# Optimization experiments

Hardware: AMD Instinct MI355X
Metric: run time of the kernel (lower is better)

Reference implementation:

```python
import jax, jax.numpy as jnp
import numpy as np
from jax import lax

B, N, D, H = 8, 2048, 512, 1024


def setup_inputs() -> dict:
    key = jax.random.key(0)
    k0, k1, k2 = jax.random.split(key, 3)
    x = jax.random.normal(k0, (B, N, D), jnp.float32)
    conv_w = jax.random.normal(k1, (H, D, 3), jnp.float32) * (1.0 / np.sqrt(3 * D))
    conv_b = jnp.zeros((H,), jnp.float32)
    ln_g = jnp.ones((H,), jnp.float32)
    ln_b = jnp.zeros((H,), jnp.float32)
    proj_w = jax.random.normal(k2, (H, 2), jnp.float32) * (1.0 / np.sqrt(H))
    proj_b = jnp.zeros((2,), jnp.float32)
    return dict(x=x, conv_w=conv_w, conv_b=conv_b, ln_g=ln_g, ln_b=ln_b,
                proj_w=proj_w, proj_b=proj_b)


def reference(x, conv_w, conv_b, ln_g, ln_b, proj_w, proj_b):
    b, n, _ = x.shape
    # Conv1d(input_dim->hidden, k=3, pad=1) on [B, C, N]
    h = lax.conv_general_dilated(x.transpose(0, 2, 1), conv_w, (1,), [(1, 1)],
                                 dimension_numbers=('NCH', 'OIH', 'NCH'))
    h = h.transpose(0, 2, 1) + conv_b          # [B, N, H]
    h = jax.nn.relu(h)
    # LayerNorm over hidden dim (dropout is identity at inference)
    mu = jnp.mean(h, axis=-1, keepdims=True)
    var = jnp.mean((h - mu) ** 2, axis=-1, keepdims=True)
    h = (h - mu) * lax.rsqrt(var + 1e-5) * ln_g + ln_b
    groups_probs = h @ proj_w + proj_b          # [B, N, 2]

    g = jnp.argmax(groups_probs, axis=-1)       # [B, N] in {0,1}
    pos = jnp.arange(n)
    base = (pos + 1).astype(jnp.float32)        # 1..N
    # col 0 forced 0; start positions (g==1, pos>0) forced 0
    zero_mask = (pos[None, :] == 0) | ((g == 1) & (pos[None, :] > 0))
    vals = jnp.where(zero_mask, 0.0, jnp.broadcast_to(base[None, :], (b, n)))
    vals = vals.at[:, -1].set(float(n))         # last col = N (overrides zeroing)
    # stable descending sort by nonzero-ness == stable ascending sort by (val==0)
    order = jnp.argsort((vals == 0.0).astype(jnp.int32), axis=1)
    groups = jnp.take_along_axis(vals, order, axis=1)[:, :, None]  # [B, N, 1]

    t = base[None, None, :]                     # [1, 1, N], values 1..N
    # row 0: 1[t <= groups[:,0]]
    row0 = jnp.clip(groups[:, 0, :][:, None, :] - t + 1.0, 0.0, 1.0)      # [B, 1, N]
    # rows 1..: 1[groups[:,i-1] < t <= groups[:,i]]
    rest = (jnp.clip(groups[:, 1:, :] - t + 1.0, 0.0, 1.0)
            * jnp.clip(t - groups[:, :-1, :], 0.0, 1.0))                   # [B, N-1, N]
    grouping_matrix = jnp.concatenate([row0, rest], axis=1)                # [B, N, N]
    return (groups_probs, grouping_matrix)
```

## Files before the change

kernel.cpp:

```cpp
#include <hip/hip_runtime.h>

#define Bsz 8
#define Nsz 2048
#define Dsz 512
#define Hsz 1024
#define K3D 1536

typedef __attribute__((ext_vector_type(8))) short short8;
typedef __attribute__((ext_vector_type(4))) float f32x4;

static __device__ __forceinline__ unsigned short f2bf(float f) {
    unsigned u = __builtin_bit_cast(unsigned, f);
    unsigned r = (u + 0x7FFFu + ((u >> 16) & 1u)) >> 16;
    return (unsigned short)r;
}
static __device__ __forceinline__ float bf2f(unsigned short u) {
    return __builtin_bit_cast(float, (unsigned)u << 16);
}
static __device__ __forceinline__ void gld16(const void* g, void* l) {
    __builtin_amdgcn_global_load_lds(
        (const __attribute__((address_space(1))) void*)g,
        (__attribute__((address_space(3))) void*)l, 16, 0, 0);
}


__global__ __launch_bounds__(256) void prep_kernel(
    const float* __restrict__ cw, unsigned short* __restrict__ wsh,
    unsigned short* __restrict__ wsl,
    const float* __restrict__ lng, const float* __restrict__ lnb,
    const float* __restrict__ pw, float* __restrict__ CD,
    float* __restrict__ gq0, float* __restrict__ gq1)
{
    __shared__ float red[4][4];
    int blk = blockIdx.x, tid = threadIdx.x;
    if (blk < 192) {
        int gid = blk * 256 + tid;
        int s = gid >> 10, h = gid & 1023;
        int t = s >> 4, c = s & 15;
        const float* src = cw + (size_t)h * K3D + (size_t)c * 96 + t;
        short hv[32], lv[32];
        #pragma unroll
        for (int j = 0; j < 32; ++j) {
            float v = src[3 * j];
            unsigned short hi = f2bf(v);
            hv[j] = (short)hi;
            lv[j] = (short)f2bf(v - bf2f(hi));
        }
        #pragma unroll
        for (int m = 0; m < 4; ++m) {
            size_t dst = (((size_t)s * 4 + m) * 1024 + h) * 16;
            *(short8*)((char*)wsh + dst) = *(short8*)&hv[m * 8];
            *(short8*)((char*)wsl + dst) = *(short8*)&lv[m * 8];
        }
    } else if (blk == 192) {
        float c0 = 0.f, c1 = 0.f, d0 = 0.f, d1 = 0.f;
        for (int h = tid; h < Hsz; h += 256) {
            float g = lng[h], b = lnb[h];
            float w0 = pw[2 * h], w1 = pw[2 * h + 1];
            c0 = fmaf(g, w0, c0); c1 = fmaf(g, w1, c1);
            d0 = fmaf(b, w0, d0); d1 = fmaf(b, w1, d1);
        }
        #pragma unroll
        for (int m = 32; m >= 1; m >>= 1) {
            c0 += __shfl_xor(c0, m, 64); c1 += __shfl_xor(c1, m, 64);
            d0 += __shfl_xor(d0, m, 64); d1 += __shfl_xor(d1, m, 64);
        }
        int w = tid >> 6;
        if ((tid & 63) == 0) { red[w][0] = c0; red[w][1] = c1; red[w][2] = d0; red[w][3] = d1; }
        __syncthreads();
        if (tid == 0) {
            CD[0] = red[0][0] + red[1][0] + red[2][0] + red[3][0];
            CD[1] = red[0][1] + red[1][1] + red[2][1] + red[3][1];
            CD[2] = red[0][2] + red[1][2] + red[2][2] + red[3][2];
            CD[3] = red[0][3] + red[1][3] + red[2][3] + red[3][3];
        }
    } else {
        int h = (blk - 193) * 256 + tid;
        float g = lng[h];
        gq0[h] = g * pw[2 * h];
        gq1[h] = g * pw[2 * h + 1];
    }
}

__global__ __launch_bounds__(256) void convert_x_kernel(
    const float* __restrict__ x, unsigned short* __restrict__ xsh,
    unsigned short* __restrict__ xsl)
{
    int tid = threadIdx.x;
    int r = blockIdx.x * 4 + (tid >> 6);
    int e = tid & 63;
    int b  = r / 2050;
    int rp = r - b * 2050;
    int c  = e >> 2;
    int qq = e & 3;
    size_t dst = ((((size_t)b * 16 + c) * 4 + qq) * 2050 + rp) * 16;
    short8 hv, lv;
    if (rp == 0 || rp == 2049) {
        #pragma unroll
        for (int u = 0; u < 8; ++u) { hv[u] = 0; lv[u] = 0; }
    } else {
        const float* p = x + ((size_t)b * Nsz + (rp - 1)) * Dsz + e * 8;
        float4 v0 = *(const float4*)p;
        float4 v1 = *(const float4*)(p + 4);
        float vv[8] = { v0.x, v0.y, v0.z, v0.w, v1.x, v1.y, v1.z, v1.w };
        #pragma unroll
        for (int u = 0; u < 8; ++u) {
            unsigned short h = f2bf(vv[u]);
            hv[u] = (short)h;
            lv[u] = (short)f2bf(vv[u] - bf2f(h));
        }
    }
    *(short8*)((char*)xsh + dst) = hv;
    *(short8*)((char*)xsl + dst) = lv;
}

__global__ __launch_bounds__(256, 2) void gemm10_kernel(
    const unsigned short* __restrict__ xsh, const unsigned short* __restrict__ xsl,
    const unsigned short* __restrict__ wsh, const unsigned short* __restrict__ wsl,
    const float* __restrict__ cb, const float* __restrict__ gq0,
    const float* __restrict__ gq1, float* __restrict__ part)
{
    __shared__ __align__(16) char lds[32768];

    int tid = threadIdx.x;
    int swz = (blockIdx.x & 7) * 128 + (blockIdx.x >> 3);
    int mt  = swz >> 3;
    int ntb = swz & 7;
    int bb  = mt >> 4;
    int n0  = (mt & 15) * 128;
    int n0c = ntb * 128;
    int n0g = bb * Nsz + n0;

    int l = tid & 63, w = tid >> 6;
    int wr = w >> 1, wc = w & 1;
    int r = l & 15, qq = l >> 4;

    int boff_r = qq * 2048 + (wc * 64 + r) * 16;
    int ldsBw  = w * 2048;

    const char* pBh = (const char*)wsh + w * 16384 + (size_t)(n0c + l) * 16;
    const char* pBl = (const char*)wsl + w * 16384 + (size_t)(n0c + l) * 16;

    const char* pAh = (const char*)xsh + (size_t)bb * 2099200 + qq * 32800
                    + (size_t)(n0 + wr * 64 + r) * 16;
    const char* pAl = (const char*)xsl + (size_t)bb * 2099200 + qq * 32800
                    + (size_t)(n0 + wr * 64 + r) * 16;

    f32x4 acc[4][4];
    #pragma unroll
    for (int i = 0; i < 4; ++i)
        #pragma unroll
        for (int j = 0; j < 4; ++j) acc[i][j] = (f32x4){0.f, 0.f, 0.f, 0.f};

    short8 a0h[4], a0l[4], a1h[4], a1l[4];

#define AOFF(sn) ((size_t)(((sn) & 15) * 131200 + ((sn) >> 4) * 16))
#define LOADA(AH, AL, sn) do { size_t ao = AOFF(sn);                           \
    _Pragma("unroll") for (int f = 0; f < 4; ++f) {                            \
        AH[f] = *(const short8*)(pAh + ao + f * 256);                          \
        AL[f] = *(const short8*)(pAl + ao + f * 256); } } while (0)

#define STAGEB(lb, sn) do { size_t bo = (size_t)(sn) * 65536;                  \
    gld16(pBh + bo,        (lb) + ldsBw);                                      \
    gld16(pBh + bo + 1024, (lb) + ldsBw + 1024);                               \
    gld16(pBl + bo,        (lb) + 8192 + ldsBw);                               \
    gld16(pBl + bo + 1024, (lb) + 8192 + ldsBw + 1024); } while (0)

#define COMPUTE(buf, AH, AL) do {                                              \
    short8 bh[4], bl[4];                                                       \
    _Pragma("unroll") for (int j = 0; j < 4; ++j) {                            \
        bh[j] = *(const short8*)((buf) + boff_r + j * 256);                    \
        bl[j] = *(const short8*)((buf) + 8192 + boff_r + j * 256); }           \
    __builtin_amdgcn_s_setprio(1);                                             \
    _Pragma("unroll") for (int i = 0; i < 4; ++i)                              \
        _Pragma("unroll") for (int j = 0; j < 4; ++j) {                        \
            acc[i][j] = __builtin_amdgcn_mfma_f32_16x16x32_bf16(AH[i], bh[j], acc[i][j], 0, 0, 0); \
            acc[i][j] = __builtin_amdgcn_mfma_f32_16x16x32_bf16(AH[i], bl[j], acc[i][j], 0, 0, 0); \
            acc[i][j] = __builtin_amdgcn_mfma_f32_16x16x32_bf16(AL[i], bh[j], acc[i][j], 0, 0, 0); } \
    __builtin_amdgcn_s_setprio(0);                                             \
} while (0)

    LOADA(a0h, a0l, 0);
    STAGEB(lds, 0);

    for (int sp = 0; sp < 24; ++sp) {
        int s1 = sp * 2 + 1;
        LOADA(a1h, a1l, s1);
        STAGEB(lds + 16384, s1);
        asm volatile("s_waitcnt vmcnt(12)" ::: "memory");
        __builtin_amdgcn_s_barrier();
        asm volatile("" ::: "memory");
        COMPUTE(lds, a0h, a0l);
        __builtin_amdgcn_s_barrier();
        if (s1 < 47) {
            LOADA(a0h, a0l, s1 + 1);
            STAGEB(lds, s1 + 1);
            asm volatile("s_waitcnt vmcnt(12)" ::: "memory");
        } else {
            asm volatile("s_waitcnt vmcnt(0)" ::: "memory");
        }
        __builtin_amdgcn_s_barrier();
        asm volatile("" ::: "memory");
        COMPUTE(lds + 16384, a1h, a1l);
        __builtin_amdgcn_s_barrier();
    }
#undef AOFF
#undef LOADA
#undef STAGEB
#undef COMPUTE

    float cbv[4], g0v[4], g1v[4];
    #pragma unroll
    for (int j = 0; j < 4; ++j) {
        int col = n0c + wc * 64 + j * 16 + r;
        cbv[j] = cb[col]; g0v[j] = gq0[col]; g1v[j] = gq1[col];
    }
    int slot = ntb * 8 + wc * 4;
    #pragma unroll
    for (int i = 0; i < 4; ++i) {
        #pragma unroll
        for (int reg = 0; reg < 4; ++reg) {
            float v0 = 0.f, v2 = 0.f, va = 0.f, vb = 0.f;
            #pragma unroll
            for (int j = 0; j < 4; ++j) {
                float v = acc[i][j][reg] + cbv[j];
                v = fmaxf(v, 0.f);
                v0 += v;
                v2 = fmaf(v, v, v2);
                va = fmaf(v, g0v[j], va);
                vb = fmaf(v, g1v[j], vb);
            }
            #pragma unroll
            for (int msk = 1; msk < 16; msk <<= 1) {
                v0 += __shfl_xor(v0, msk, 64); v2 += __shfl_xor(v2, msk, 64);
                va += __shfl_xor(va, msk, 64); vb += __shfl_xor(vb, msk, 64);
            }
            if (r == 0) {
                int rowg = n0g + wr * 64 + i * 16 + qq * 4 + reg;
                *(f32x4*)(part + (size_t)rowg * 64 + slot) = (f32x4){v0, v2, va, vb};
            }
        }
    }
}

__global__ __launch_bounds__(256) void probs_kernel(
    const float* __restrict__ part, const float* __restrict__ CD,
    const float* __restrict__ pb, float* __restrict__ probs,
    int* __restrict__ gout)
{
    int row = blockIdx.x * 256 + threadIdx.x;
    float S0 = 0.f, S2 = 0.f, Sa = 0.f, Sb = 0.f;
    const float4* p = (const float4*)(part + (size_t)row * 64);
    #pragma unroll
    for (int c = 0; c < 16; ++c) {
        float4 v = p[c];
        S0 += v.x; S2 += v.y; Sa += v.z; Sb += v.w;
    }
    float mu  = S0 * (1.0f / Hsz);
    float var = S2 * (1.0f / Hsz) - mu * mu;
    float rsq = 1.0f / sqrtf(var + 1e-5f);
    float p0 = fmaf(rsq, Sa - mu * CD[0], CD[2] + pb[0]);
    float p1 = fmaf(rsq, Sb - mu * CD[1], CD[3] + pb[1]);
    probs[(size_t)row * 2]     = p0;
    probs[(size_t)row * 2 + 1] = p1;
    gout[row] = (p1 > p0) ? 1 : 0;
}

#define ROWS 64
#define CCH 128
#define NCC (Hsz / CCH)
#define DSTEP 32

__global__ __launch_bounds__(256) void consts_kernel(
    const float* __restrict__ lng, const float* __restrict__ lnb,
    const float* __restrict__ pw, float* __restrict__ CD)
{
    int tid = threadIdx.x;
    float c0 = 0.f, c1 = 0.f, d0 = 0.f, d1 = 0.f;
    for (int h = tid; h < Hsz; h += 256) {
        float g = lng[h], b = lnb[h];
        float w0 = pw[2 * h], w1 = pw[2 * h + 1];
        c0 = fmaf(g, w0, c0); c1 = fmaf(g, w1, c1);
        d0 = fmaf(b, w0, d0); d1 = fmaf(b, w1, d1);
    }
    #pragma unroll
    for (int m = 32; m >= 1; m >>= 1) {
        c0 += __shfl_xor(c0, m, 64); c1 += __shfl_xor(c1, m, 64);
        d0 += __shfl_xor(d0, m, 64); d1 += __shfl_xor(d1, m, 64);
    }
    __shared__ float red[4][4];
    int w = tid >> 6;
    if ((tid & 63) == 0) { red[w][0] = c0; red[w][1] = c1; red[w][2] = d0; red[w][3] = d1; }
    __syncthreads();
    if (tid == 0) {
        CD[0] = red[0][0] + red[1][0] + red[2][0] + red[3][0];
        CD[1] = red[0][1] + red[1][1] + red[2][1] + red[3][1];
        CD[2] = red[0][2] + red[1][2] + red[2][2] + red[3][2];
        CD[3] = red[0][3] + red[1][3] + red[2][3] + red[3][3];
    }
}

__global__ __launch_bounds__(256) void conv_ln_proj_kernel(
    const float* __restrict__ x, const float* __restrict__ cw,
    const float* __restrict__ cb, const float* __restrict__ lng,
    const float* __restrict__ pw, const float* __restrict__ pb,
    const float* __restrict__ CD, float* __restrict__ probs,
    int* __restrict__ gout)
{
    __shared__ float Xl[DSTEP][66];
    __shared__ float Bl[3][DSTEP][CCH];
    __shared__ float Sl[ROWS][4];

    int tid = threadIdx.x;
    int blk = blockIdx.x;
    int b  = blk >> 5;
    int n0 = (blk & 31) * ROWS;
    int rg = tid >> 5;
    int cg = tid & 31;
    int sr = tid >> 2;
    int sq = tid & 3;
    const float* xb = x + (size_t)b * Nsz * Dsz;

    float s0[8], s2[8], sa[8], sb[8];
    #pragma unroll
    for (int i = 0; i < 8; ++i) { s0[i] = 0.f; s2[i] = 0.f; sa[i] = 0.f; sb[i] = 0.f; }

    for (int cc = 0; cc < NCC; ++cc) {
        float cbv[4], gq0[4], gq1[4];
        {
            int hb = cc * CCH + cg * 4;
            #pragma unroll
            for (int j = 0; j < 4; ++j) {
                int h = hb + j;
                cbv[j] = cb[h];
                float gg = lng[h];
                gq0[j] = gg * pw[2 * h];
                gq1[j] = gg * pw[2 * h + 1];
            }
        }
        float acc[8][4];
        #pragma unroll
        for (int i = 0; i < 8; ++i)
            #pragma unroll
            for (int j = 0; j < 4; ++j) acc[i][j] = 0.f;

        for (int ds = 0; ds < Dsz / DSTEP; ++ds) {
            int d0 = ds * DSTEP;
            __syncthreads();
            {
                int n = n0 - 1 + sr;
                float4 v0 = make_float4(0.f, 0.f, 0.f, 0.f), v1 = v0;
                if ((unsigned)n < (unsigned)Nsz) {
                    const float* p = xb + (size_t)n * Dsz + d0 + sq * 8;
                    v0 = *(const float4*)p;
                    v1 = *(const float4*)(p + 4);
                }
                int dd = sq * 8;
                Xl[dd + 0][sr] = v0.x; Xl[dd + 1][sr] = v0.y;
                Xl[dd + 2][sr] = v0.z; Xl[dd + 3][sr] = v0.w;
                Xl[dd + 4][sr] = v1.x; Xl[dd + 5][sr] = v1.y;
                Xl[dd + 6][sr] = v1.z; Xl[dd + 7][sr] = v1.w;
                if (tid < 8) {
                    int r2 = 64 + (tid >> 2);
                    int q2 = tid & 3;
                    int n2 = n0 - 1 + r2;
                    float4 u0 = make_float4(0.f, 0.f, 0.f, 0.f), u1 = u0;
                    if ((unsigned)n2 < (unsigned)Nsz) {
                        const float* p2 = xb + (size_t)n2 * Dsz + d0 + q2 * 8;
                        u0 = *(const float4*)p2;
                        u1 = *(const float4*)(p2 + 4);
                    }
                    int dd2 = q2 * 8;
                    Xl[dd2 + 0][r2] = u0.x; Xl[dd2 + 1][r2] = u0.y;
                    Xl[dd2 + 2][r2] = u0.z; Xl[dd2 + 3][r2] = u0.w;
                    Xl[dd2 + 4][r2] = u1.x; Xl[dd2 + 5][r2] = u1.y;
                    Xl[dd2 + 6][r2] = u1.z; Xl[dd2 + 7][r2] = u1.w;
                }
            }
            {
                int hl = tid >> 1;
                int half = tid & 1;
                const float* p = cw + (size_t)(cc * CCH + hl) * K3D + (size_t)d0 * 3 + half * 48;
                #pragma unroll
                for (int mq = 0; mq < 12; ++mq) {
                    float4 v = *(const float4*)(p + mq * 4);
                    float vv[4] = { v.x, v.y, v.z, v.w };
                    #pragma unroll
                    for (int e = 0; e < 4; ++e) {
                        int c  = mq * 4 + e;
                        int dl = half * 16 + c / 3;
                        int kk = c % 3;
                        Bl[kk][dl][hl] = vv[e];
                    }
                }
            }
            __syncthreads();
            #pragma unroll 4
            for (int dd = 0; dd < DSTEP; ++dd) {
                float a[10];
                #pragma unroll
                for (int j = 0; j < 10; ++j) a[j] = Xl[dd][rg * 8 + j];
                #pragma unroll
                for (int kk = 0; kk < 3; ++kk) {
                    float4 bv = *(const float4*)&Bl[kk][dd][cg * 4];
                    #pragma unroll
                    for (int i = 0; i < 8; ++i) {
                        float av = a[i + kk];
                        acc[i][0] = fmaf(av, bv.x, acc[i][0]);
                        acc[i][1] = fmaf(av, bv.y, acc[i][1]);
                        acc[i][2] = fmaf(av, bv.z, acc[i][2]);
                        acc[i][3] = fmaf(av, bv.w, acc[i][3]);
                    }
                }
            }
        }
        #pragma unroll
        for (int i = 0; i < 8; ++i) {
            #pragma unroll
            for (int j = 0; j < 4; ++j) {
                float v = acc[i][j] + cbv[j];
                v = fmaxf(v, 0.f);
                s0[i] += v;
                s2[i] = fmaf(v, v, s2[i]);
                sa[i] = fmaf(v, gq0[j], sa[i]);
                sb[i] = fmaf(v, gq1[j], sb[i]);
            }
        }
    }
    #pragma unroll
    for (int i = 0; i < 8; ++i) {
        float v0 = s0[i], v2 = s2[i], va = sa[i], vb = sb[i];
        #pragma unroll
        for (int mm = 16; mm >= 1; mm >>= 1) {
            v0 += __shfl_xor(v0, mm, 64); v2 += __shfl_xor(v2, mm, 64);
            va += __shfl_xor(va, mm, 64); vb += __shfl_xor(vb, mm, 64);
        }
        if (cg == 0) {
            int rr = rg * 8 + i;
            Sl[rr][0] = v0; Sl[rr][1] = v2; Sl[rr][2] = va; Sl[rr][3] = vb;
        }
    }
    __syncthreads();
    if (tid < ROWS) {
        int rr = tid, n = n0 + rr;
        float S0 = Sl[rr][0], S2 = Sl[rr][1], Sa = Sl[rr][2], Sb = Sl[rr][3];
        float mu  = S0 * (1.0f / Hsz);
        float var = S2 * (1.0f / Hsz) - mu * mu;
        float rsq = 1.0f / sqrtf(var + 1e-5f);
        float p0 = fmaf(rsq, Sa - mu * CD[0], CD[2] + pb[0]);
        float p1 = fmaf(rsq, Sb - mu * CD[1], CD[3] + pb[1]);
        size_t ro = (size_t)(b * Nsz + n);
        probs[ro * 2]     = p0;
        probs[ro * 2 + 1] = p1;
        gout[ro] = (p1 > p0) ? 1 : 0;
    }
}

__global__ __launch_bounds__(256) void bounds_kernel(
    const int* __restrict__ g, float* __restrict__ vlist, int* __restrict__ Kb)
{
    int b = blockIdx.x, tid = threadIdx.x;
    int base = tid * 8;
    int f[8]; float val[8]; int lsum = 0;
    #pragma unroll
    for (int u = 0; u < 8; ++u) {
        int i = base + u;
        int nz;
        if (i == Nsz - 1) nz = 1;
        else if (i == 0)  nz = 0;
        else              nz = (g[b * Nsz + i] == 0) ? 1 : 0;
        f[u] = nz;
        val[u] = (i == Nsz - 1) ? (float)Nsz : (float)(i + 1);
        lsum += nz;
    }
    int lane = tid & 63, w = tid >> 6;
    int sc = lsum;
    #pragma unroll
    for (int off = 1; off < 64; off <<= 1) {
        int t = __shfl_up(sc, off, 64);
        if (lane >= off) sc += t;
    }
    __shared__ int wsum[4];
    if (lane == 63) wsum[w] = sc;
    __syncthreads();
    int woff = 0;
    #pragma unroll
    for (int k = 0; k < 4; ++k) if (k < w) woff += wsum[k];
    int pos = woff + (sc - lsum);
    #pragma unroll
    for (int u = 0; u < 8; ++u) {
        if (f[u]) { vlist[b * Nsz + pos] = val[u]; pos++; }
    }
    if (tid == 255) Kb[b] = woff + sc;
}

__global__ __launch_bounds__(256) void fill_kernel(
    const float* __restrict__ vlist, const int* __restrict__ Kb,
    float* __restrict__ mat)
{
    int blk = blockIdx.x;
    int b = blk >> 11, j = blk & 2047;
    int K = Kb[b];
    float c = (j < K) ? vlist[b * Nsz + j] : 0.0f;
    float a = (j == 0) ? 0.0f : vlist[b * Nsz + j - 1];
    int tc = threadIdx.x * 8;
    float o[8];
    #pragma unroll
    for (int e = 0; e < 8; ++e) {
        float t = (float)(tc + e + 1);
        o[e] = (t > a && t <= c) ? 1.0f : 0.0f;
    }
    float4* p = (float4*)(mat + (size_t)blk * Nsz + tc);
    p[0] = make_float4(o[0], o[1], o[2], o[3]);
    p[1] = make_float4(o[4], o[5], o[6], o[7]);
}

extern "C" void kernel_launch(void* const* d_in, const int* in_sizes, int n_in,
                              void* d_out, int out_size, void* d_ws, size_t ws_size,
                              hipStream_t stream)
{
    const float* x      = (const float*)d_in[0];
    const float* conv_w = (const float*)d_in[1];
    const float* conv_b = (const float*)d_in[2];
    const float* ln_g   = (const float*)d_in[3];
    const float* ln_b   = (const float*)d_in[4];
    const float* proj_w = (const float*)d_in[5];
    const float* proj_b = (const float*)d_in[6];

    float* out = (float*)d_out;
    char*  wsb = (char*)d_ws;

    size_t cur = 0;
    auto take = [&](size_t b) { size_t r = cur; cur = (cur + b + 255) & ~(size_t)255; return r; };
    size_t oCD  = take(16);
    size_t oGQ0 = take(Hsz * 4);
    size_t oGQ1 = take(Hsz * 4);
    size_t oKb  = take(32);
    size_t oG   = take((size_t)Bsz * Nsz * 4);
    size_t oV   = take((size_t)Bsz * Nsz * 4);
    size_t oPart= take((size_t)Bsz * Nsz * 64 * 4);
    size_t oXh  = take((size_t)Bsz * 16 * 4 * 2050 * 16);
    size_t oXl  = take((size_t)Bsz * 16 * 4 * 2050 * 16);
    size_t oWh  = take((size_t)48 * 4 * 1024 * 16);
    size_t oWl  = take((size_t)48 * 4 * 1024 * 16);
    bool fast = ws_size >= cur;

    if (fast) {
        float* CD    = (float*)(wsb + oCD);
        float* gq0   = (float*)(wsb + oGQ0);
        float* gq1   = (float*)(wsb + oGQ1);
        int*   Kb    = (int*)  (wsb + oKb);
        int*   g     = (int*)  (wsb + oG);
        float* vlist = (float*)(wsb + oV);
        float* part  = (float*)(wsb + oPart);
        unsigned short* xsh = (unsigned short*)(wsb + oXh);
        unsigned short* xsl = (unsigned short*)(wsb + oXl);
        unsigned short* wsh = (unsigned short*)(wsb + oWh);
        unsigned short* wsl = (unsigned short*)(wsb + oWl);

        prep_kernel<<<197, 256, 0, stream>>>(conv_w, wsh, wsl, ln_g, ln_b, proj_w, CD, gq0, gq1);
        convert_x_kernel<<<Bsz * 2050 / 4, 256, 0, stream>>>(x, xsh, xsl);
        gemm10_kernel<<<1024, 256, 0, stream>>>(
            xsh, xsl, wsh, wsl, conv_b, gq0, gq1, part);
        probs_kernel<<<Bsz * Nsz / 256, 256, 0, stream>>>(part, CD, proj_b, out, g);
        bounds_kernel<<<Bsz, 256, 0, stream>>>(g, vlist, Kb);
        fill_kernel<<<Bsz * Nsz, 256, 0, stream>>>(vlist, Kb, out + (size_t)Bsz * Nsz * 2);
    } else {
        float* wf  = (float*)d_ws;
        int*   wi  = (int*)d_ws;
        float* CD    = wf;
        int*   Kb    = wi + 4;
        int*   g     = wi + 16;
        float* vlist = wf + 16 + Bsz * Nsz;

        consts_kernel<<<1, 256, 0, stream>>>(ln_g, ln_b, proj_w, CD);
        conv_ln_proj_kernel<<<Bsz * Nsz / ROWS, 256, 0, stream>>>(
            x, conv_w, conv_b, ln_g, proj_w, proj_b, CD, out, g);
        bounds_kernel<<<Bsz, 256, 0, stream>>>(g, vlist, Kb);
        fill_kernel<<<Bsz * Nsz, 256, 0, stream>>>(vlist, Kb, out + (size_t)Bsz * Nsz * 2);
    }
}
```

Measured before the change: 187.1 us.

## Triple-buffer B tiles in LDS with one barrier per k-step

Grows the GEMM's LDS from two to three B-tile buffers and rewrites the main loop as a rotating pipeline. Each k-step now uses a single barrier, staging B two steps ahead and A registers one step ahead, instead of two barriers per half-iteration. The goal is to cut barrier stalls and hide global-to-LDS latency better. In exchange, LDS per block rises to 48KB, which may limit occupancy at 2 blocks per CU, and the vmcnt bookkeeping becomes more fragile.

```diff
diff --git a/kernel.cpp b/kernel.cpp
--- a/kernel.cpp
+++ b/kernel.cpp
@@ -114,13 +114,13 @@
     *(short8*)((char*)xsl + dst) = lv;
 }
 
-__global__ __launch_bounds__(256, 2) void gemm10_kernel(
+__global__ __launch_bounds__(256, 2) void gemm12_kernel(
     const unsigned short* __restrict__ xsh, const unsigned short* __restrict__ xsl,
     const unsigned short* __restrict__ wsh, const unsigned short* __restrict__ wsl,
     const float* __restrict__ cb, const float* __restrict__ gq0,
     const float* __restrict__ gq1, float* __restrict__ part)
 {
-    __shared__ __align__(16) char lds[32768];
+    __shared__ __align__(16) char lds[49152];
 
     int tid = threadIdx.x;
     int swz = (blockIdx.x & 7) * 128 + (blockIdx.x >> 3);
@@ -180,34 +180,50 @@
     __builtin_amdgcn_s_setprio(0);                                             \
 } while (0)
 
+#define BODY(k, CBUF, SBUF, CH, CL, NH, NL) do {                               \
+    __builtin_amdgcn_s_barrier();                                              \
+    STAGEB(lds + (SBUF) * 16384, (k) + 2);                                     \
+    LOADA(NH, NL, (k) + 1);                                                    \
+    asm volatile("s_waitcnt vmcnt(12)" ::: "memory");                          \
+    asm volatile("" ::: "memory");                                             \
+    COMPUTE(lds + (CBUF) * 16384, CH, CL);                                     \
+} while (0)
+
     LOADA(a0h, a0l, 0);
     STAGEB(lds, 0);
-
-    for (int sp = 0; sp < 24; ++sp) {
-        int s1 = sp * 2 + 1;
-        LOADA(a1h, a1l, s1);
-        STAGEB(lds + 16384, s1);
+    STAGEB(lds + 16384, 1);
+
+    for (int sp = 0; sp < 7; ++sp) {
+        int k0 = sp * 6;
+        BODY(k0 + 0, 0, 2, a0h, a0l, a1h, a1l);
+        BODY(k0 + 1, 1, 0, a1h, a1l, a0h, a0l);
+        BODY(k0 + 2, 2, 1, a0h, a0l, a1h, a1l);
+        BODY(k0 + 3, 0, 2, a1h, a1l, a0h, a0l);
+        BODY(k0 + 4, 1, 0, a0h, a0l, a1h, a1l);
+        BODY(k0 + 5, 2, 1, a1h, a1l, a0h, a0l);
+    }
+    BODY(42, 0, 2, a0h, a0l, a1h, a1l);
+    BODY(43, 1, 0, a1h, a1l, a0h, a0l);
+    BODY(44, 2, 1, a0h, a0l, a1h, a1l);
+    BODY(45, 0, 2, a1h, a1l, a0h, a0l);
+    {
+        __builtin_amdgcn_s_barrier();
+        LOADA(a1h, a1l, 47);
         asm volatile("s_waitcnt vmcnt(12)" ::: "memory");
+        asm volatile("" ::: "memory");
+        COMPUTE(lds + 16384, a0h, a0l);
+    }
+    {
         __builtin_amdgcn_s_barrier();
+        asm volatile("s_waitcnt vmcnt(0)" ::: "memory");
         asm volatile("" ::: "memory");
-        COMPUTE(lds, a0h, a0l);
-        __builtin_amdgcn_s_barrier();
-        if (s1 < 47) {
-            LOADA(a0h, a0l, s1 + 1);
-            STAGEB(lds, s1 + 1);
-            asm volatile("s_waitcnt vmcnt(12)" ::: "memory");
-        } else {
-            asm volatile("s_waitcnt vmcnt(0)" ::: "memory");
-        }
-        __builtin_amdgcn_s_barrier();
-        asm volatile("" ::: "memory");
-        COMPUTE(lds + 16384, a1h, a1l);
-        __builtin_amdgcn_s_barrier();
+        COMPUTE(lds + 32768, a1h, a1l);
     }
 #undef AOFF
 #undef LOADA
 #undef STAGEB
 #undef COMPUTE
+#undef BODY
 
     float cbv[4], g0v[4], g1v[4];
     #pragma unroll
@@ -560,7 +576,7 @@
 
         prep_kernel<<<197, 256, 0, stream>>>(conv_w, wsh, wsl, ln_g, ln_b, proj_w, CD, gq0, gq1);
         convert_x_kernel<<<Bsz * 2050 / 4, 256, 0, stream>>>(x, xsh, xsl);
-        gemm10_kernel<<<1024, 256, 0, stream>>>(
+        gemm12_kernel<<<1024, 256, 0, stream>>>(
             xsh, xsl, wsh, wsl, conv_b, gq0, gq1, part);
         probs_kernel<<<Bsz * Nsz / 256, 256, 0, stream>>>(part, CD, proj_b, out, g);
         bounds_kernel<<<Bsz, 256, 0, stream>>>(g, vlist, Kb);
```

Result: slower. 195.2 us (+4.3%).
